# Kernel optimization log

Hardware: AMD Instinct MI355X
Metric: run time of the kernel (lower is better)

The kernel has to match this reference:

```python
import jax, jax.numpy as jnp
import numpy as np

N_NODES = 100000
N_EDGES = 800000
IN_DIM = 128
NUM_HEADS = 8
HEAD_DIM = 16  # out_dim // num_heads = 128 // 8


def setup_inputs() -> dict:
    key = jax.random.key(0)
    ks = jax.random.split(key, 10)
    scale = 1.0 / np.sqrt(IN_DIM)
    return {
        "x": jax.random.normal(ks[0], (N_NODES, IN_DIM), dtype=jnp.float32),
        "edge_index": jax.random.randint(ks[1], (2, N_EDGES), 0, N_NODES, dtype=jnp.int64),
        "virt_h": jax.random.normal(ks[2], (1, IN_DIM), dtype=jnp.float32),
        "virt_edge_index": jax.random.randint(ks[3], (2, 1), 0, 1, dtype=jnp.int64),
        "Wq": jax.random.normal(ks[4], (IN_DIM, NUM_HEADS * HEAD_DIM), dtype=jnp.float32) * scale,
        "bq": jnp.zeros((NUM_HEADS * HEAD_DIM,), dtype=jnp.float32),
        "Wk": jax.random.normal(ks[5], (IN_DIM, NUM_HEADS * HEAD_DIM), dtype=jnp.float32) * scale,
        "bk": jnp.zeros((NUM_HEADS * HEAD_DIM,), dtype=jnp.float32),
        "Wv": jax.random.normal(ks[6], (IN_DIM, NUM_HEADS * HEAD_DIM), dtype=jnp.float32) * scale,
        "bv": jnp.zeros((NUM_HEADS * HEAD_DIM,), dtype=jnp.float32),
    }


def reference(x, edge_index, virt_h, virt_edge_index, Wq, bq, Wk, bk, Wv, bv):
    # use_virt_nodes=False: virt_h / virt_edge_index are unused dummies.
    n = x.shape[0]
    H, D = NUM_HEADS, HEAD_DIM
    Q = (x @ Wq + bq).reshape(n, H, D)
    K = (x @ Wk + bk).reshape(n, H, D)
    V = (x @ Wv + bv).reshape(n, H, D)

    src = edge_index[0]
    dst = edge_index[1]

    # edge-wise gather QK dot -> clamp -> exp; score: [E, H, 1]
    dot = jnp.sum(K[src] * Q[dst], axis=-1, keepdims=True) / np.sqrt(D).astype(np.float32)
    score = jnp.exp(jnp.clip(dot, -5.0, 5.0))

    msg = V[src] * score  # [E, H, D]
    wV = jax.ops.segment_sum(msg, dst, num_segments=n)     # [N, H, D]
    Z = jax.ops.segment_sum(score, dst, num_segments=n)    # [N, H, 1]

    h_out = (wV / (Z + 1e-6)).reshape(n, H * D)
    return h_out
```

## Files before the change

### kernel.cpp

```cpp
#include <hip/hip_runtime.h>

#define IN_DIM   128
#define NH       8
#define HD       16
#define OUTD     128
#define QKVD     384
#define SH       7

typedef unsigned short ushort_t;
typedef unsigned int   uint_t;
typedef __bf16 bf16x8 __attribute__((ext_vector_type(8)));
typedef float  f32x4  __attribute__((ext_vector_type(4)));

__device__ __forceinline__ float bf2f(ushort_t u) {
    return __uint_as_float(((uint_t)u) << 16);
}
__device__ __forceinline__ ushort_t f2bf(float f) {
    uint_t u = __float_as_uint(f);
    u += 0x7FFFu + ((u >> 16) & 1u);
    return (ushort_t)(u >> 16);
}

__global__ __launch_bounds__(256) void prep_w(
    const float* __restrict__ Wq, const float* __restrict__ Wk,
    const float* __restrict__ Wv, ushort_t* __restrict__ Wt,
    unsigned long long* __restrict__ desc)
{
    __shared__ float ld[32][33];
    int mat  = blockIdx.x >> 4;
    int tile = blockIdx.x & 15;
    int k0 = (tile >> 2) * 32, c0 = (tile & 3) * 32;
    const float* W = (mat == 0) ? Wq : (mat == 1) ? Wk : Wv;
    int t = threadIdx.x;
    {
        int k = t >> 3, c4 = (t & 7) * 4;
        float4 f = *(const float4*)&W[(size_t)(k0 + k) * 128 + c0 + c4];
        ld[k][c4 + 0] = f.x; ld[k][c4 + 1] = f.y;
        ld[k][c4 + 2] = f.z; ld[k][c4 + 3] = f.w;
    }
    __syncthreads();
    {
        int c = t >> 3, kg = (t & 7) * 4;
        union { ushort_t h[4]; uint2 u; } o;
        o.h[0] = f2bf(ld[kg + 0][c]); o.h[1] = f2bf(ld[kg + 1][c]);
        o.h[2] = f2bf(ld[kg + 2][c]); o.h[3] = f2bf(ld[kg + 3][c]);
        *(uint2*)&Wt[((size_t)(mat * 128 + c0 + c)) * 128 + k0 + kg] = o.u;
    }
    int t0 = blockIdx.x * 256 + threadIdx.x;
    if (t0 < 128) desc[t0] = 0ULL;
}

__global__ __launch_bounds__(256) void ehist(
    const int* __restrict__ ei, int* __restrict__ Hf, int E, int NBC)
{
    __shared__ int lh[1024];
    for (int i = threadIdx.x; i < 1024; i += 256) lh[i] = 0;
    __syncthreads();
    int CH = (E + 127) >> 7;
    int e0 = blockIdx.x * CH;
    int e1 = min(E, e0 + CH);
    for (int e = e0 + threadIdx.x; e < e1; e += 256)
        atomicAdd(&lh[ei[E + e] >> SH], 1);
    __syncthreads();
    for (int b = threadIdx.x; b < NBC; b += 256)
        Hf[b * 128 + blockIdx.x] = lh[b];
}

__global__ __launch_bounds__(1024) void scan_onepass(
    int* __restrict__ P, unsigned long long* __restrict__ desc, int N)
{
    __shared__ int sdata[1024];
    __shared__ int s_prefix;
    int b = blockIdx.x;
    int i = b * 1024 + threadIdx.x;
    int v = (i < N) ? P[i] : 0;
    sdata[threadIdx.x] = v;
    __syncthreads();
    for (int off = 1; off < 1024; off <<= 1) {
        int t = (threadIdx.x >= off) ? sdata[threadIdx.x - off] : 0;
        __syncthreads();
        sdata[threadIdx.x] += t;
        __syncthreads();
    }
    int incl  = sdata[threadIdx.x];
    int total = sdata[1023];

    if (threadIdx.x == 0) {
        unsigned long long st1 = ((unsigned long long)((b == 0) ? 2 : 1) << 32)
                                 | (uint_t)total;
        __hip_atomic_store(&desc[b], st1, __ATOMIC_RELEASE, __HIP_MEMORY_SCOPE_AGENT);
        int prefix = 0;
        if (b > 0) {
            int bb = b - 1;
            for (;;) {
                unsigned long long d = __hip_atomic_load(
                    &desc[bb], __ATOMIC_ACQUIRE, __HIP_MEMORY_SCOPE_AGENT);
                uint_t st = (uint_t)(d >> 32);
                if (st == 0) continue;
                prefix += (int)(uint_t)(d & 0xFFFFFFFFu);
                if (st == 2) break;
                bb--;
            }
            __hip_atomic_store(&desc[b],
                ((unsigned long long)2 << 32) | (uint_t)(prefix + total),
                __ATOMIC_RELEASE, __HIP_MEMORY_SCOPE_AGENT);
        }
        s_prefix = prefix;
    }
    __syncthreads();
    if (i < N) P[i] = s_prefix + incl - v;
}

__global__ __launch_bounds__(256) void ebucket(
    const int* __restrict__ ei, const int* __restrict__ S,
    uint_t* __restrict__ bkt, int E, int NBC)
{
    __shared__ int lb[1024];
    for (int b = threadIdx.x; b < NBC; b += 256)
        lb[b] = S[b * 128 + blockIdx.x];
    __syncthreads();
    int CH = (E + 127) >> 7;
    int e0 = blockIdx.x * CH;
    int e1 = min(E, e0 + CH);
    for (int e = e0 + threadIdx.x; e < e1; e += 256) {
        int d   = ei[E + e];
        int src = ei[e];
        int pos = atomicAdd(&lb[d >> SH], 1);
        bkt[pos] = (uint_t)src | ((uint_t)(d & 127) << 20);
    }
}

__global__ __launch_bounds__(256) void efine(
    const uint_t* __restrict__ bkt, const int* __restrict__ S,
    int* __restrict__ P, int* __restrict__ sorted_src,
    int E, int N, int NBC)
{
    __shared__ int cnt[128];
    __shared__ int scn[128];
    int b    = blockIdx.x;
    int base = S[b * 128];
    int end  = (b + 1 < NBC) ? S[(b + 1) * 128] : E;
    int m    = end - base;
    if (threadIdx.x < 128) cnt[threadIdx.x] = 0;
    __syncthreads();
    for (int i = threadIdx.x; i < m; i += 256)
        atomicAdd(&cnt[bkt[base + i] >> 20], 1);
    __syncthreads();
    if (threadIdx.x < 128) scn[threadIdx.x] = cnt[threadIdx.x];
    __syncthreads();
    for (int off = 1; off < 128; off <<= 1) {
        int v = (threadIdx.x >= off && threadIdx.x < 128) ? scn[threadIdx.x - off] : 0;
        __syncthreads();
        if (threadIdx.x < 128) scn[threadIdx.x] += v;
        __syncthreads();
    }
    if (threadIdx.x < 128) {
        int excl = scn[threadIdx.x] - cnt[threadIdx.x];
        int n = b * 128 + threadIdx.x;
        if (n < N) P[n] = base + excl;
        cnt[threadIdx.x] = excl;
    }
    __syncthreads();
    for (int i = threadIdx.x; i < m; i += 256) {
        uint_t r = bkt[base + i];
        int pos = atomicAdd(&cnt[r >> 20], 1);
        sorted_src[base + pos] = (int)(r & 0xFFFFFu);
    }
}

__global__ __launch_bounds__(384, 3) void gemm(
    const float* __restrict__ x, const ushort_t* __restrict__ Wt,
    const float* __restrict__ bq, const float* __restrict__ bk,
    const float* __restrict__ bv,
    ushort_t* __restrict__ qkv,
    int N, int ntiles)
{
    __shared__ ushort_t sh[8320];

    const int tid  = threadIdx.x;
    const int w    = tid >> 6;
    const int quad = (tid >> 4) & 3;
    const int l15  = tid & 15;
    const int colg = w << 6;

    bf16x8 bfr[4][4];
#pragma unroll
    for (int kt = 0; kt < 4; kt++)
#pragma unroll
        for (int cs = 0; cs < 4; cs++) {
            int col = colg + cs * 16 + l15;
            bfr[kt][cs] = *(const bf16x8*)&Wt[(size_t)col * 128 + kt * 32 + quad * 8];
        }

    const int mat = w >> 1;
    const float* Bp = (mat == 0) ? bq : (mat == 1) ? bk : bv;
    float bias[4];
#pragma unroll
    for (int cs = 0; cs < 4; cs++)
        bias[cs] = Bp[((w & 1) << 6) + cs * 16 + l15];

    for (int tile = blockIdx.x; tile < ntiles; tile += gridDim.x) {
        const int row0 = tile * 64;
        __syncthreads();

        for (int ch = tid; ch < 1024; ch += 384) {
            int row = ch >> 4;
            int kc  = ch & 15;
            int grow = row0 + row; if (grow > N - 1) grow = N - 1;
            const float* xp = x + (size_t)grow * IN_DIM + kc * 8;
            float4 f0 = *(const float4*)xp;
            float4 f1 = *(const float4*)(xp + 4);
            union { ushort_t h[8]; uint4 u; } tt;
            tt.h[0] = f2bf(f0.x); tt.h[1] = f2bf(f0.y);
            tt.h[2] = f2bf(f0.z); tt.h[3] = f2bf(f0.w);
            tt.h[4] = f2bf(f1.x); tt.h[5] = f2bf(f1.y);
            tt.h[6] = f2bf(f1.z); tt.h[7] = f2bf(f1.w);
            *(uint4*)&sh[(kc * 65 + row) * 8] = tt.u;
        }
        __syncthreads();

        f32x4 acc[4][4];
#pragma unroll
        for (int r = 0; r < 4; r++)
#pragma unroll
            for (int cs = 0; cs < 4; cs++) acc[r][cs] = (f32x4){0.f, 0.f, 0.f, 0.f};

#pragma unroll
        for (int kt = 0; kt < 4; kt++) {
            int kc = kt * 4 + quad;
            bf16x8 af[4];
#pragma unroll
            for (int r = 0; r < 4; r++)
                af[r] = *(const bf16x8*)&sh[(kc * 65 + r * 16 + l15) * 8];
#pragma unroll
            for (int r = 0; r < 4; r++)
#pragma unroll
                for (int cs = 0; cs < 4; cs++)
                    acc[r][cs] = __builtin_amdgcn_mfma_f32_16x16x32_bf16(
                        af[r], bfr[kt][cs], acc[r][cs], 0, 0, 0);
        }

#define EPS 392
#pragma unroll
        for (int qq = 0; qq < 4; qq++) {
            __syncthreads();
            int lrow = quad << 2;
#pragma unroll
            for (int cs = 0; cs < 4; cs++) {
                int col = (w << 6) + cs * 16 + l15;
#pragma unroll
                for (int reg = 0; reg < 4; reg++)
                    sh[(lrow + reg) * EPS + col] = f2bf(acc[qq][cs][reg] + bias[cs]);
            }
            __syncthreads();
#pragma unroll
            for (int i = 0; i < 2; i++) {
                int c = tid + i * 384;
                int row = c / 48;
                int col = (c % 48) * 8;
                int grow = row0 + qq * 16 + row;
                if (grow < N) {
                    uint4 val = *(const uint4*)&sh[row * EPS + col];
                    *(uint4*)&qkv[(size_t)grow * QKVD + col] = val;
                }
            }
        }
#undef EPS
    }
}

__global__ __launch_bounds__(256) void segment_attn(
    const ushort_t* __restrict__ qkv,
    const int* __restrict__ P, const int* __restrict__ sorted_src,
    float* __restrict__ out, int N, int E)
{
    int n = (blockIdx.x * 256 + threadIdx.x) >> 4;
    int g = threadIdx.x & 15;
    if (n >= N) return;
    int start = P[n];
    int end   = (n + 1 < N) ? P[n + 1] : E;
    int deg   = end - start;

    const uint_t* qrow = (const uint_t*)(qkv + (size_t)n * QKVD);
    uint4 qu = *(const uint4*)(qrow + g * 4);
    float q0 = bf2f((ushort_t)(qu.x & 0xFFFF)), q1 = bf2f((ushort_t)(qu.x >> 16));
    float q2 = bf2f((ushort_t)(qu.y & 0xFFFF)), q3 = bf2f((ushort_t)(qu.y >> 16));
    float q4 = bf2f((ushort_t)(qu.z & 0xFFFF)), q5 = bf2f((ushort_t)(qu.z >> 16));
    float q6 = bf2f((ushort_t)(qu.w & 0xFFFF)), q7 = bf2f((ushort_t)(qu.w >> 16));

    float a0 = 0.f, a1 = 0.f, a2 = 0.f, a3 = 0.f;
    float a4 = 0.f, a5 = 0.f, a6 = 0.f, a7 = 0.f, z = 0.f;

    int myidx = (g < deg) ? sorted_src[start + g] : 0;
    int wbase = (threadIdx.x & 63) & 48;

#define PROC(ku, vu)                                                       \
    {                                                                      \
        float p = bf2f((ushort_t)((ku).x & 0xFFFF)) * q0                   \
                + bf2f((ushort_t)((ku).x >> 16))    * q1                   \
                + bf2f((ushort_t)((ku).y & 0xFFFF)) * q2                   \
                + bf2f((ushort_t)((ku).y >> 16))    * q3                   \
                + bf2f((ushort_t)((ku).z & 0xFFFF)) * q4                   \
                + bf2f((ushort_t)((ku).z >> 16))    * q5                   \
                + bf2f((ushort_t)((ku).w & 0xFFFF)) * q6                   \
                + bf2f((ushort_t)((ku).w >> 16))    * q7;                  \
        p += __shfl_xor(p, 1);                                             \
        p = fminf(fmaxf(p * 0.25f, -5.f), 5.f);                            \
        float s = __expf(p);                                               \
        a0 += bf2f((ushort_t)((vu).x & 0xFFFF)) * s;                       \
        a1 += bf2f((ushort_t)((vu).x >> 16))    * s;                       \
        a2 += bf2f((ushort_t)((vu).y & 0xFFFF)) * s;                       \
        a3 += bf2f((ushort_t)((vu).y >> 16))    * s;                       \
        a4 += bf2f((ushort_t)((vu).z & 0xFFFF)) * s;                       \
        a5 += bf2f((ushort_t)((vu).z >> 16))    * s;                       \
        a6 += bf2f((ushort_t)((vu).w & 0xFFFF)) * s;                       \
        a7 += bf2f((ushort_t)((vu).w >> 16))    * s;                       \
        z += s;                                                            \
    }

    int cnt = (deg < 16) ? deg : 16;
    int t = 0;
    for (; t + 2 <= cnt; t += 2) {
        int s0 = __shfl(myidx, wbase + t);
        int s1 = __shfl(myidx, wbase + t + 1);
        const uint_t* kv0 = (const uint_t*)(qkv + (size_t)s0 * QKVD + 128);
        const uint_t* kv1 = (const uint_t*)(qkv + (size_t)s1 * QKVD + 128);
        uint4 ku0 = *(const uint4*)(kv0 + g * 4);
        uint4 ku1 = *(const uint4*)(kv1 + g * 4);
        uint4 vu0 = *(const uint4*)(kv0 + 64 + g * 4);
        uint4 vu1 = *(const uint4*)(kv1 + 64 + g * 4);
        PROC(ku0, vu0); PROC(ku1, vu1);
    }
    if (t < cnt) {
        int s0 = __shfl(myidx, wbase + t);
        const uint_t* kv0 = (const uint_t*)(qkv + (size_t)s0 * QKVD + 128);
        uint4 ku0 = *(const uint4*)(kv0 + g * 4);
        uint4 vu0 = *(const uint4*)(kv0 + 64 + g * 4);
        PROC(ku0, vu0);
    }
    for (int j = start + 16; j < end; j++) {
        int s0 = sorted_src[j];
        const uint_t* kv0 = (const uint_t*)(qkv + (size_t)s0 * QKVD + 128);
        uint4 ku0 = *(const uint4*)(kv0 + g * 4);
        uint4 vu0 = *(const uint4*)(kv0 + 64 + g * 4);
        PROC(ku0, vu0);
    }
#undef PROC

    float inv = 1.f / (z + 1e-6f);
    float4 o0 = {a0 * inv, a1 * inv, a2 * inv, a3 * inv};
    float4 o1 = {a4 * inv, a5 * inv, a6 * inv, a7 * inv};
    float* ob = out + (size_t)n * OUTD + g * 8;
    *(float4*)ob = o0;
    *(float4*)(ob + 4) = o1;
}

extern "C" void kernel_launch(void* const* d_in, const int* in_sizes, int n_in,
                              void* d_out, int out_size, void* d_ws, size_t ws_size,
                              hipStream_t stream) {
    const float* x  = (const float*)d_in[0];
    const int*   ei = (const int*)d_in[1];
    const float* Wq = (const float*)d_in[4];
    const float* bq = (const float*)d_in[5];
    const float* Wk = (const float*)d_in[6];
    const float* bk = (const float*)d_in[7];
    const float* Wv = (const float*)d_in[8];
    const float* bv = (const float*)d_in[9];
    float* out = (float*)d_out;

    const int N = in_sizes[0] / IN_DIM;
    const int E = in_sizes[1] / 2;
    const int NBC = (N + 127) >> 7;
    const int NS  = NBC * 128;

    char* wsb = (char*)d_ws;
    ushort_t* qkv = (ushort_t*)wsb;
    ushort_t* Wt  = qkv + (size_t)N * QKVD;
    int* Hf = (int*)(Wt + 384 * 128);
    unsigned long long* desc = (unsigned long long*)(Hf + NS);
    int* sorted = (int*)((char*)desc + 1024);
    uint_t* bkt = (uint_t*)(sorted + E);
    int* P = (int*)(bkt + E);

    const int ntiles = (N + 63) / 64;
    const int NB     = (NS + 1023) / 1024;

    prep_w<<<48, 256, 0, stream>>>(Wq, Wk, Wv, Wt, desc);
    ehist<<<128, 256, 0, stream>>>(ei, Hf, E, NBC);
    scan_onepass<<<NB, 1024, 0, stream>>>(Hf, desc, NS);
    ebucket<<<128, 256, 0, stream>>>(ei, Hf, bkt, E, NBC);
    efine<<<NBC, 256, 0, stream>>>(bkt, Hf, P, sorted, E, N, NBC);
    gemm<<<512, 384, 0, stream>>>(x, Wt, bq, bk, bv, qkv, N, ntiles);
    segment_attn<<<((size_t)N * 16 + 255) / 256, 256, 0, stream>>>(
        qkv, P, sorted, out, N, E);
}
```

Measured before the change: 272.4 us.

## Restructure counting sort into locally-sorted regions with staged fine pass

Merges the histogram and bucket-scatter kernels into one kernel where each of 64 blocks sorts its edge chunk locally in shared memory by coarse bucket and writes contiguous regions. The global scan now processes four entries per thread, and the fine pass gathers each bucket's slices from the 64 regions into shared memory, sorts there, and writes sorted_src coalesced. This removes one launch and replaces random global scatters with coalesced writes. The attention kernel also unrolls its edge loops to four and two and uses nontemporal output stores. The 64-block sort pass gives low parallelism and uses large shared buffers, and the fixed 4096-entry staging buffer assumes a bounded bucket size.

After: 248.8 us. 8.7% less time.

```diff
diff --git a/kernel.cpp b/kernel.cpp
--- a/kernel.cpp
+++ b/kernel.cpp
@@ -6,6 +6,7 @@
 #define OUTD     128
 #define QKVD     384
 #define SH       7
+#define NSORTB   64
 
 typedef unsigned short ushort_t;
 typedef unsigned int   uint_t;
@@ -50,31 +51,61 @@
     if (t0 < 128) desc[t0] = 0ULL;
 }
 
-__global__ __launch_bounds__(256) void ehist(
-    const int* __restrict__ ei, int* __restrict__ Hf, int E, int NBC)
-{
-    __shared__ int lh[1024];
-    for (int i = threadIdx.x; i < 1024; i += 256) lh[i] = 0;
-    __syncthreads();
-    int CH = (E + 127) >> 7;
-    int e0 = blockIdx.x * CH;
-    int e1 = min(E, e0 + CH);
-    for (int e = e0 + threadIdx.x; e < e1; e += 256)
-        atomicAdd(&lh[ei[E + e] >> SH], 1);
-    __syncthreads();
-    for (int b = threadIdx.x; b < NBC; b += 256)
-        Hf[b * 128 + blockIdx.x] = lh[b];
-}
-
-__global__ __launch_bounds__(1024) void scan_onepass(
-    int* __restrict__ P, unsigned long long* __restrict__ desc, int N)
+__global__ __launch_bounds__(1024) void ebucketA(
+    const int* __restrict__ ei, int* __restrict__ Hf, int* __restrict__ aux,
+    uint_t* __restrict__ regions, int E, int NBC, int CH)
+{
+    __shared__ uint_t recs[12500];
+    __shared__ int hist[1024];
+    __shared__ int scn[1024];
+    const int tid = threadIdx.x;
+    const int blk = blockIdx.x;
+    const int e0g = blk * CH;
+    const int e1g = min(E, e0g + CH);
+    const int m   = e1g - e0g;
+
+    hist[tid] = 0;
+    __syncthreads();
+    for (int e = e0g + tid; e < e1g; e += 1024)
+        atomicAdd(&hist[ei[E + e] >> SH], 1);
+    __syncthreads();
+    for (int b = tid; b < NBC; b += 1024)
+        Hf[b * NSORTB + blk] = hist[b];
+    scn[tid] = hist[tid];
+    __syncthreads();
+    for (int off = 1; off < 1024; off <<= 1) {
+        int v = (tid >= off) ? scn[tid - off] : 0;
+        __syncthreads();
+        scn[tid] += v;
+        __syncthreads();
+    }
+    int excl = scn[tid] - hist[tid];
+    if (tid < NBC) aux[tid * NSORTB + blk] = excl;
+    if (tid == 0)  aux[NBC * NSORTB + blk] = m;
+    hist[tid] = excl;
+    __syncthreads();
+    for (int e = e0g + tid; e < e1g; e += 1024) {
+        int d = ei[E + e];
+        int src = ei[e];
+        int slot = atomicAdd(&hist[d >> SH], 1);
+        recs[slot] = (uint_t)src | ((uint_t)(d & 127) << 20);
+    }
+    __syncthreads();
+    for (int s = tid; s < m; s += 1024)
+        regions[(size_t)blk * CH + s] = recs[s];
+}
+
+__global__ __launch_bounds__(1024) void scan4(
+    int* __restrict__ P, unsigned long long* __restrict__ desc, int NS)
 {
     __shared__ int sdata[1024];
     __shared__ int s_prefix;
-    int b = blockIdx.x;
-    int i = b * 1024 + threadIdx.x;
-    int v = (i < N) ? P[i] : 0;
-    sdata[threadIdx.x] = v;
+    int b  = blockIdx.x;
+    int i0 = (b * 1024 + threadIdx.x) * 4;
+    int4 v = {0, 0, 0, 0};
+    if (i0 < NS) v = *(const int4*)&P[i0];
+    int s = v.x + v.y + v.z + v.w;
+    sdata[threadIdx.x] = s;
     __syncthreads();
     for (int off = 1; off < 1024; off <<= 1) {
         int t = (threadIdx.x >= off) ? sdata[threadIdx.x - off] : 0;
@@ -108,64 +139,85 @@
         s_prefix = prefix;
     }
     __syncthreads();
-    if (i < N) P[i] = s_prefix + incl - v;
-}
-
-__global__ __launch_bounds__(256) void ebucket(
-    const int* __restrict__ ei, const int* __restrict__ S,
-    uint_t* __restrict__ bkt, int E, int NBC)
-{
-    __shared__ int lb[1024];
-    for (int b = threadIdx.x; b < NBC; b += 256)
-        lb[b] = S[b * 128 + blockIdx.x];
-    __syncthreads();
-    int CH = (E + 127) >> 7;
-    int e0 = blockIdx.x * CH;
-    int e1 = min(E, e0 + CH);
-    for (int e = e0 + threadIdx.x; e < e1; e += 256) {
-        int d   = ei[E + e];
-        int src = ei[e];
-        int pos = atomicAdd(&lb[d >> SH], 1);
-        bkt[pos] = (uint_t)src | ((uint_t)(d & 127) << 20);
+    if (i0 < NS) {
+        int base = s_prefix + incl - s;
+        int4 o;
+        o.x = base;
+        o.y = base + v.x;
+        o.z = base + v.x + v.y;
+        o.w = base + v.x + v.y + v.z;
+        *(int4*)&P[i0] = o;
     }
 }
 
 __global__ __launch_bounds__(256) void efine(
-    const uint_t* __restrict__ bkt, const int* __restrict__ S,
+    const uint_t* __restrict__ regions, const int* __restrict__ aux,
+    const int* __restrict__ S,
     int* __restrict__ P, int* __restrict__ sorted_src,
-    int E, int N, int NBC)
-{
-    __shared__ int cnt[128];
-    __shared__ int scn[128];
-    int b    = blockIdx.x;
-    int base = S[b * 128];
-    int end  = (b + 1 < NBC) ? S[(b + 1) * 128] : E;
-    int m    = end - base;
-    if (threadIdx.x < 128) cnt[threadIdx.x] = 0;
-    __syncthreads();
-    for (int i = threadIdx.x; i < m; i += 256)
-        atomicAdd(&cnt[bkt[base + i] >> 20], 1);
-    __syncthreads();
-    if (threadIdx.x < 128) scn[threadIdx.x] = cnt[threadIdx.x];
+    int N, int NBC, int CH)
+{
+    __shared__ int rl[64], ro[64], doff[64];
+    __shared__ int cnt[128], scn2[128];
+    __shared__ uint_t stage[4096];
+    __shared__ int    sst[4096];
+    const int tid = threadIdx.x;
+    const int b   = blockIdx.x;
+    const int base = S[b * NSORTB];
+
+    if (tid < 64) {
+        int r0 = aux[b * NSORTB + tid];
+        int r1 = aux[(b + 1) * NSORTB + tid];
+        ro[tid] = r0;
+        rl[tid] = r1 - r0;
+        doff[tid] = r1 - r0;
+    }
+    __syncthreads();
+    for (int off = 1; off < 64; off <<= 1) {
+        int v = (tid >= off && tid < 64) ? doff[tid - off] : 0;
+        __syncthreads();
+        if (tid < 64) doff[tid] += v;
+        __syncthreads();
+    }
+    const int m = doff[63];
+
+    {
+        int r = tid >> 2, k = tid & 3;
+        int dst0 = doff[r] - rl[r];
+        int src0 = ro[r];
+        int len  = rl[r];
+        for (int i = k; i < len; i += 4)
+            stage[dst0 + i] = regions[(size_t)r * CH + src0 + i];
+    }
+    __syncthreads();
+
+    if (tid < 128) cnt[tid] = 0;
+    __syncthreads();
+    for (int i = tid; i < m; i += 256)
+        atomicAdd(&cnt[stage[i] >> 20], 1);
+    __syncthreads();
+    if (tid < 128) scn2[tid] = cnt[tid];
     __syncthreads();
     for (int off = 1; off < 128; off <<= 1) {
-        int v = (threadIdx.x >= off && threadIdx.x < 128) ? scn[threadIdx.x - off] : 0;
-        __syncthreads();
-        if (threadIdx.x < 128) scn[threadIdx.x] += v;
-        __syncthreads();
-    }
-    if (threadIdx.x < 128) {
-        int excl = scn[threadIdx.x] - cnt[threadIdx.x];
-        int n = b * 128 + threadIdx.x;
+        int v = (tid >= off && tid < 128) ? scn2[tid - off] : 0;
+        __syncthreads();
+        if (tid < 128) scn2[tid] += v;
+        __syncthreads();
+    }
+    if (tid < 128) {
+        int excl = scn2[tid] - cnt[tid];
+        int n = b * 128 + tid;
         if (n < N) P[n] = base + excl;
-        cnt[threadIdx.x] = excl;
-    }
-    __syncthreads();
-    for (int i = threadIdx.x; i < m; i += 256) {
-        uint_t r = bkt[base + i];
+        cnt[tid] = excl;
+    }
+    __syncthreads();
+    for (int i = tid; i < m; i += 256) {
+        uint_t r = stage[i];
         int pos = atomicAdd(&cnt[r >> 20], 1);
-        sorted_src[base + pos] = (int)(r & 0xFFFFFu);
-    }
+        sst[pos] = (int)(r & 0xFFFFFu);
+    }
+    __syncthreads();
+    for (int i = tid; i < m; i += 256)
+        sorted_src[base + i] = sst[i];
 }
 
 __global__ __launch_bounds__(384, 3) void gemm(
@@ -320,6 +372,25 @@
 
     int cnt = (deg < 16) ? deg : 16;
     int t = 0;
+    for (; t + 4 <= cnt; t += 4) {
+        int s0 = __shfl(myidx, wbase + t);
+        int s1 = __shfl(myidx, wbase + t + 1);
+        int s2 = __shfl(myidx, wbase + t + 2);
+        int s3 = __shfl(myidx, wbase + t + 3);
+        const uint_t* kv0 = (const uint_t*)(qkv + (size_t)s0 * QKVD + 128);
+        const uint_t* kv1 = (const uint_t*)(qkv + (size_t)s1 * QKVD + 128);
+        const uint_t* kv2 = (const uint_t*)(qkv + (size_t)s2 * QKVD + 128);
+        const uint_t* kv3 = (const uint_t*)(qkv + (size_t)s3 * QKVD + 128);
+        uint4 ku0 = *(const uint4*)(kv0 + g * 4);
+        uint4 ku1 = *(const uint4*)(kv1 + g * 4);
+        uint4 ku2 = *(const uint4*)(kv2 + g * 4);
+        uint4 ku3 = *(const uint4*)(kv3 + g * 4);
+        uint4 vu0 = *(const uint4*)(kv0 + 64 + g * 4);
+        uint4 vu1 = *(const uint4*)(kv1 + 64 + g * 4);
+        uint4 vu2 = *(const uint4*)(kv2 + 64 + g * 4);
+        uint4 vu3 = *(const uint4*)(kv3 + 64 + g * 4);
+        PROC(ku0, vu0); PROC(ku1, vu1); PROC(ku2, vu2); PROC(ku3, vu3);
+    }
     for (; t + 2 <= cnt; t += 2) {
         int s0 = __shfl(myidx, wbase + t);
         int s1 = __shfl(myidx, wbase + t + 1);
@@ -338,8 +409,19 @@
         uint4 vu0 = *(const uint4*)(kv0 + 64 + g * 4);
         PROC(ku0, vu0);
     }
-    for (int j = start + 16; j < end; j++) {
+    for (int j = start + 16; j + 2 <= end; j += 2) {
         int s0 = sorted_src[j];
+        int s1 = sorted_src[j + 1];
+        const uint_t* kv0 = (const uint_t*)(qkv + (size_t)s0 * QKVD + 128);
+        const uint_t* kv1 = (const uint_t*)(qkv + (size_t)s1 * QKVD + 128);
+        uint4 ku0 = *(const uint4*)(kv0 + g * 4);
+        uint4 ku1 = *(const uint4*)(kv1 + g * 4);
+        uint4 vu0 = *(const uint4*)(kv0 + 64 + g * 4);
+        uint4 vu1 = *(const uint4*)(kv1 + 64 + g * 4);
+        PROC(ku0, vu0); PROC(ku1, vu1);
+    }
+    if (deg > 16 && ((deg - 16) & 1)) {
+        int s0 = sorted_src[end - 1];
         const uint_t* kv0 = (const uint_t*)(qkv + (size_t)s0 * QKVD + 128);
         uint4 ku0 = *(const uint4*)(kv0 + g * 4);
         uint4 vu0 = *(const uint4*)(kv0 + 64 + g * 4);
@@ -348,11 +430,11 @@
 #undef PROC
 
     float inv = 1.f / (z + 1e-6f);
-    float4 o0 = {a0 * inv, a1 * inv, a2 * inv, a3 * inv};
-    float4 o1 = {a4 * inv, a5 * inv, a6 * inv, a7 * inv};
+    f32x4 o0 = {a0 * inv, a1 * inv, a2 * inv, a3 * inv};
+    f32x4 o1 = {a4 * inv, a5 * inv, a6 * inv, a7 * inv};
     float* ob = out + (size_t)n * OUTD + g * 8;
-    *(float4*)ob = o0;
-    *(float4*)(ob + 4) = o1;
+    __builtin_nontemporal_store(o0, (f32x4*)ob);
+    __builtin_nontemporal_store(o1, (f32x4*)(ob + 4));
 }
 
 extern "C" void kernel_launch(void* const* d_in, const int* in_sizes, int n_in,
@@ -371,25 +453,26 @@
     const int N = in_sizes[0] / IN_DIM;
     const int E = in_sizes[1] / 2;
     const int NBC = (N + 127) >> 7;
-    const int NS  = NBC * 128;
+    const int NS  = NBC * NSORTB;
+    const int CH  = (E + NSORTB - 1) / NSORTB;
 
     char* wsb = (char*)d_ws;
     ushort_t* qkv = (ushort_t*)wsb;
     ushort_t* Wt  = qkv + (size_t)N * QKVD;
     int* Hf = (int*)(Wt + 384 * 128);
     unsigned long long* desc = (unsigned long long*)(Hf + NS);
-    int* sorted = (int*)((char*)desc + 1024);
-    uint_t* bkt = (uint_t*)(sorted + E);
-    int* P = (int*)(bkt + E);
+    int* aux = (int*)((char*)desc + 1024);
+    uint_t* regions = (uint_t*)(aux + (NBC + 1) * NSORTB);
+    int* sorted = (int*)(regions + (size_t)NSORTB * CH);
+    int* P = sorted + E;
 
     const int ntiles = (N + 63) / 64;
-    const int NB     = (NS + 1023) / 1024;
+    const int NSB    = (NS + 4095) / 4096;
 
     prep_w<<<48, 256, 0, stream>>>(Wq, Wk, Wv, Wt, desc);
-    ehist<<<128, 256, 0, stream>>>(ei, Hf, E, NBC);
-    scan_onepass<<<NB, 1024, 0, stream>>>(Hf, desc, NS);
-    ebucket<<<128, 256, 0, stream>>>(ei, Hf, bkt, E, NBC);
-    efine<<<NBC, 256, 0, stream>>>(bkt, Hf, P, sorted, E, N, NBC);
+    ebucketA<<<NSORTB, 1024, 0, stream>>>(ei, Hf, aux, regions, E, NBC, CH);
+    scan4<<<NSB, 1024, 0, stream>>>(Hf, desc, NS);
+    efine<<<NBC, 256, 0, stream>>>(regions, aux, Hf, P, sorted, N, NBC, CH);
     gemm<<<512, 384, 0, stream>>>(x, Wt, bq, bk, bv, qkv, N, ntiles);
     segment_attn<<<((size_t)N * 16 + 255) / 256, 256, 0, stream>>>(
         qkv, P, sorted, out, N, E);
```
